# Optimization experiments

Hardware: AMD Instinct MI355X
Metric: run time of the kernel (lower is better)

## Reference

```python
import jax, jax.numpy as jnp
import numpy as np

HEAD_DIM = 512 // (8 * 2)  # in_dim // (num_heads * 2) = 32
SQRT2 = np.sqrt(2.0).astype(np.float32)


def dwt1d_haar(x):
    # Haar DWT along last dim: L=(even+odd)/sqrt2, H=(even-odd)/sqrt2
    xe, xo = x[..., 0::2], x[..., 1::2]
    return (xe + xo) / SQRT2, (xe - xo) / SQRT2


def idwt1d_haar(L, H):
    # Inverse: even=(L+H)/sqrt2, odd=(L-H)/sqrt2, interleaved
    even = (L + H) / SQRT2
    odd = (L - H) / SQRT2
    x = jnp.stack([even, odd], axis=-1)  # [..., D/2, 2]
    return x.reshape(*x.shape[:-2], -1)  # [..., D]


def setup_inputs() -> dict:
    key = jax.random.key(0)
    k1, k2, k3, k4 = jax.random.split(key, 4)
    B, S, D = 8, 2048, 512
    queries = jax.random.normal(k1, (B, S, D), dtype=jnp.float32)
    keys = jax.random.normal(k2, (B, S, D), dtype=jnp.float32)
    values = jax.random.normal(k3, (B, S, D), dtype=jnp.float32)
    W_o = jax.random.normal(k4, (D, D), dtype=jnp.float32) * (1.0 / np.sqrt(D))
    b_o = jnp.zeros((D,), dtype=jnp.float32)
    return {"queries": queries, "keys": keys, "values": values, "W_o": W_o, "b_o": b_o}


def reference(queries, keys, values, W_o, b_o):
    scale = 1.0 / jnp.sqrt(jnp.asarray(HEAD_DIM, dtype=queries.dtype))
    q_L, q_H = dwt1d_haar(queries)
    k_L, k_H = dwt1d_haar(keys)
    v_L, v_H = dwt1d_haar(values)
    # [B,S,S] score matrices for each wavelet branch
    attn_L = jax.nn.softmax(jnp.einsum("bqd,bkd->bqk", q_L, k_L) * scale, axis=-1)
    attn_H = jax.nn.softmax(jnp.einsum("bqd,bkd->bqk", q_H, k_H) * scale, axis=-1)
    L_out = jnp.einsum("bqk,bkd->bqd", attn_L, v_L)
    H_out = jnp.einsum("bqk,bkd->bqd", attn_H, v_H)
    output = idwt1d_haar(L_out, H_out)  # [B,S,D]
    return output @ W_o.T + b_o
```

## Files before the change

kernel.cpp:

```cpp
#include <hip/hip_runtime.h>

#define INV_SQRT2 0.70710678118654752f
#define QSCALE    0.17677669529663689f
#define LOG2E     1.44269504088896340f
#define SM_SHIFT  32.0f

typedef __attribute__((ext_vector_type(8))) short bf16x8;
typedef __attribute__((ext_vector_type(4))) float f32x4;
typedef __attribute__((ext_vector_type(16))) float f32x16;

__device__ __forceinline__ unsigned pack2bf(float a, float b) {
  union { float f; unsigned u; } ua, ub; ua.f = a; ub.f = b;
  unsigned ra = ua.u + 0x7FFFu + ((ua.u >> 16) & 1u);
  unsigned rb = ub.u + 0x7FFFu + ((ub.u >> 16) & 1u);
  return __builtin_amdgcn_perm(rb, ra, 0x07060302);
}

__device__ __forceinline__ float exp2_raw(float x) {
  float r;
  asm("v_exp_f32 %0, %1" : "=v"(r) : "v"(x));
  return r;
}

__device__ __forceinline__ void async16(const short* g, short* l) {
  typedef __attribute__((address_space(3))) unsigned lds_u32;
  typedef const __attribute__((address_space(1))) unsigned glb_u32;
  __builtin_amdgcn_global_load_lds((glb_u32*)g, (lds_u32*)l, 16, 0, 0);
}

__global__ void dwt_all(const float* __restrict__ q, const float* __restrict__ k,
                        const float* __restrict__ v, const float* __restrict__ W,
                        short* __restrict__ qs, short* __restrict__ ks,
                        short* __restrict__ vt, short* __restrict__ w2) {
  __shared__ float tL[64][65];
  __shared__ float tH[64][65];
  int bi = blockIdx.x;
  int t = threadIdx.x;
  if (bi < 2048) {
    int idx = bi * 256 + t;
    int j = idx & 31;
    int s = (idx >> 5) & 2047;
    int b = idx >> 16;
    const float4* qp = (const float4*)(q + ((size_t)(b * 2048 + s)) * 512 + j * 16);
    const float4* kp = (const float4*)(k + ((size_t)(b * 2048 + s)) * 512 + j * 16);
    float4 a0 = qp[0], a1 = qp[1], a2 = qp[2], a3 = qp[3];
    float4 c0 = kp[0], c1 = kp[1], c2 = kp[2], c3 = kp[3];
    union { bf16x8 v; unsigned u[4]; } qL, qH, kL, kH;
    const float cs = INV_SQRT2 * QSCALE * LOG2E;
    qL.u[0] = pack2bf((a0.x + a0.y) * cs, (a0.z + a0.w) * cs);
    qL.u[1] = pack2bf((a1.x + a1.y) * cs, (a1.z + a1.w) * cs);
    qL.u[2] = pack2bf((a2.x + a2.y) * cs, (a2.z + a2.w) * cs);
    qL.u[3] = pack2bf((a3.x + a3.y) * cs, (a3.z + a3.w) * cs);
    qH.u[0] = pack2bf((a0.x - a0.y) * cs, (a0.z - a0.w) * cs);
    qH.u[1] = pack2bf((a1.x - a1.y) * cs, (a1.z - a1.w) * cs);
    qH.u[2] = pack2bf((a2.x - a2.y) * cs, (a2.z - a2.w) * cs);
    qH.u[3] = pack2bf((a3.x - a3.y) * cs, (a3.z - a3.w) * cs);
    kL.u[0] = pack2bf((c0.x + c0.y) * INV_SQRT2, (c0.z + c0.w) * INV_SQRT2);
    kL.u[1] = pack2bf((c1.x + c1.y) * INV_SQRT2, (c1.z + c1.w) * INV_SQRT2);
    kL.u[2] = pack2bf((c2.x + c2.y) * INV_SQRT2, (c2.z + c2.w) * INV_SQRT2);
    kL.u[3] = pack2bf((c3.x + c3.y) * INV_SQRT2, (c3.z + c3.w) * INV_SQRT2);
    kH.u[0] = pack2bf((c0.x - c0.y) * INV_SQRT2, (c0.z - c0.w) * INV_SQRT2);
    kH.u[1] = pack2bf((c1.x - c1.y) * INV_SQRT2, (c1.z - c1.w) * INV_SQRT2);
    kH.u[2] = pack2bf((c2.x - c2.y) * INV_SQRT2, (c2.z - c2.w) * INV_SQRT2);
    kH.u[3] = pack2bf((c3.x - c3.y) * INV_SQRT2, (c3.z - c3.w) * INV_SQRT2);
    size_t oL = ((size_t)(b * 2) * 2048 + s) * 256 + j * 8;
    size_t oH = oL + (size_t)2048 * 256;
    *(bf16x8*)(qs + oL) = qL.v;  *(bf16x8*)(qs + oH) = qH.v;
    *(bf16x8*)(ks + oL) = kL.v;  *(bf16x8*)(ks + oH) = kH.v;
  } else if (bi < 3072) {
    int bi2 = bi - 2048;
    int it = bi2 & 3, st = (bi2 >> 2) & 31, b = bi2 >> 7;
#pragma unroll
    for (int rep = 0; rep < 8; rep++) {
      int unit = rep * 256 + t;
      int r = unit >> 5, cp = (unit & 31) * 2;
      float4 vv = *(const float4*)(v + ((size_t)(b * 2048 + st * 64 + r)) * 512 + it * 128 + cp * 2);
      tL[r][cp]     = (vv.x + vv.y) * INV_SQRT2;
      tL[r][cp + 1] = (vv.z + vv.w) * INV_SQRT2;
      tH[r][cp]     = (vv.x - vv.y) * INV_SQRT2;
      tH[r][cp + 1] = (vv.z - vv.w) * INV_SQRT2;
    }
    __syncthreads();
#pragma unroll
    for (int rep = 0; rep < 2; rep++) {
      int unit = rep * 256 + t;
      int i = unit >> 3, cc = unit & 7;
      union { bf16x8 v; unsigned u[4]; } pL, pH;
#pragma unroll
      for (int p = 0; p < 4; p++) {
        pL.u[p] = pack2bf(tL[cc * 8 + p * 2][i], tL[cc * 8 + p * 2 + 1][i]);
        pH.u[p] = pack2bf(tH[cc * 8 + p * 2][i], tH[cc * 8 + p * 2 + 1][i]);
      }
      size_t o = ((size_t)(b * 2) * 256 + it * 64 + i) * 2048 + st * 64 + cc * 8;
      *(bf16x8*)(vt + o) = pL.v;
      *(bf16x8*)(vt + o + (size_t)256 * 2048) = pH.v;
    }
  } else {
    int idx = (bi - 3072) * 256 + t;
    int j = idx >> 6, i4 = (idx & 63) * 4;
    const float4* src = (const float4*)(W + (size_t)j * 512 + 2 * i4);
    float4 f0 = src[0], f1 = src[1];
    uint2 dl, dh;
    dl.x = pack2bf((f0.x + f0.y) * INV_SQRT2, (f0.z + f0.w) * INV_SQRT2);
    dl.y = pack2bf((f1.x + f1.y) * INV_SQRT2, (f1.z + f1.w) * INV_SQRT2);
    dh.x = pack2bf((f0.x - f0.y) * INV_SQRT2, (f0.z - f0.w) * INV_SQRT2);
    dh.y = pack2bf((f1.x - f1.y) * INV_SQRT2, (f1.z - f1.w) * INV_SQRT2);
    *(uint2*)(w2 + (size_t)j * 512 + i4) = dl;
    *(uint2*)(w2 + (size_t)j * 512 + 256 + i4) = dh;
  }
}

__launch_bounds__(256, 2)
__global__ void flash_attn(const short* __restrict__ qs, const short* __restrict__ ks,
                           const short* __restrict__ vt, short* __restrict__ os) {
  __shared__ short lds[36864];
  short* klds = lds;
  short* vlds = lds + 16384;
  short* plds = lds + 32768;

  int tid = threadIdx.x;
  int w = tid >> 6, L = tid & 63;
  int lq = L & 31, hi = L >> 5;
  int qt = w & 1, ct = w >> 1;
  int bb = blockIdx.x, qb = blockIdx.y;

  bf16x8 qf[16];
  const short* qptr = qs + (((size_t)bb * 2048) + qb * 64 + qt * 32 + lq) * 256 + hi * 8;
#pragma unroll
  for (int ksI = 0; ksI < 16; ksI++)
    qf[ksI] = *(const bf16x8*)(qptr + ksI * 16);

  f32x16 oacc[4];
#pragma unroll
  for (int mt = 0; mt < 4; mt++)
#pragma unroll
    for (int i = 0; i < 16; i++) oacc[mt][i] = 0.f;
  float l_i = 0.f;

  const short* kbase = ks + ((size_t)bb * 2048) * 256;
  const short* vbase = vt + ((size_t)bb * 256) * 2048;

  int krow = ct * 32 + lq, ksw = krow & 7;
  int qrow = qt * 32 + lq, qsw = qrow & 7;
  int sw8 = lq & 7;

  const short* kaddr[16];
#pragma unroll
  for (int i = 0; i < 16; i++)
    kaddr[i] = klds + krow * 256 + (((i << 1) | hi) ^ ksw) * 8;
  short* pwr[4];
#pragma unroll
  for (int g = 0; g < 4; g++)
    pwr[g] = plds + qrow * 64 + ((4 * ct + g) ^ qsw) * 8 + hi * 4;
  const short* prdA[4];
  const short* prdB[4];
#pragma unroll
  for (int i = 0; i < 4; i++) {
    int ch = (((i << 1) | hi) ^ sw8) * 8;
    prdA[i] = plds + lq * 64 + ch;
    prdB[i] = plds + (32 + lq) * 64 + ch;
  }
  int vch[4];
#pragma unroll
  for (int i = 0; i < 4; i++)
    vch[i] = (((i << 1) | hi) ^ sw8) * 8;
  const short* vrowp[2];
#pragma unroll
  for (int dt = 0; dt < 2; dt++)
    vrowp[dt] = vlds + (w * 64 + dt * 32 + lq) * 64;

  const short* kp[8];
  const short* vp[8];
#pragma unroll
  for (int rep = 0; rep < 8; rep++) {
    int o = w * 8 + rep;
    int r = 2 * o + (L >> 5);
    int c = (L & 31) ^ (r & 7);
    kp[rep] = kbase + r * 256 + c * 8;
    int n = 8 * o + (L >> 3);
    int cv = (L & 7) ^ (n & 7);
    vp[rep] = vbase + n * 2048 + cv * 8;
  }

#pragma unroll
  for (int rep = 0; rep < 8; rep++) {
    async16(kp[rep], klds + (w * 8 + rep) * 512);
    kp[rep] += 16384;
  }
  __syncthreads();

  for (int kt = 0; kt < 32; kt++) {
#pragma unroll
    for (int rep = 0; rep < 8; rep++) {
      async16(vp[rep], vlds + (w * 8 + rep) * 512);
      vp[rep] += 64;
    }

    f32x16 s0, s1;
#pragma unroll
    for (int i = 0; i < 16; i++) { s0[i] = 0.f; s1[i] = 0.f; }
#pragma unroll
    for (int ksI = 0; ksI < 16; ksI += 2) {
      bf16x8 kb0 = *(const bf16x8*)kaddr[ksI];
      bf16x8 kb1 = *(const bf16x8*)kaddr[ksI + 1];
      s0 = __builtin_amdgcn_mfma_f32_32x32x16_bf16(kb0, qf[ksI], s0, 0, 0, 0);
      s1 = __builtin_amdgcn_mfma_f32_32x32x16_bf16(kb1, qf[ksI + 1], s1, 0, 0, 0);
    }

    float rs = 0.f;
#pragma unroll
    for (int g = 0; g < 4; g++) {
      float p0 = exp2_raw(s0[4 * g]     + s1[4 * g]     - SM_SHIFT);
      float p1 = exp2_raw(s0[4 * g + 1] + s1[4 * g + 1] - SM_SHIFT);
      float p2 = exp2_raw(s0[4 * g + 2] + s1[4 * g + 2] - SM_SHIFT);
      float p3 = exp2_raw(s0[4 * g + 3] + s1[4 * g + 3] - SM_SHIFT);
      rs += (p0 + p1) + (p2 + p3);
      uint2 d; d.x = pack2bf(p0, p1); d.y = pack2bf(p2, p3);
      *(uint2*)pwr[g] = d;
    }
    l_i += rs;
    __syncthreads();

    if (kt < 31) {
#pragma unroll
      for (int rep = 0; rep < 8; rep++) {
        async16(kp[rep], klds + (w * 8 + rep) * 512);
        kp[rep] += 16384;
      }
    }

    bf16x8 pa[4], pb[4];
#pragma unroll
    for (int i = 0; i < 4; i++) {
      pa[i] = *(const bf16x8*)prdA[i];
      pb[i] = *(const bf16x8*)prdB[i];
    }
#pragma unroll
    for (int dt = 0; dt < 2; dt++) {
#pragma unroll
      for (int i = 0; i < 4; i++) {
        bf16x8 vb = *(const bf16x8*)(vrowp[dt] + vch[i]);
        oacc[dt * 2]     = __builtin_amdgcn_mfma_f32_32x32x16_bf16(vb, pa[i], oacc[dt * 2], 0, 0, 0);
        oacc[dt * 2 + 1] = __builtin_amdgcn_mfma_f32_32x32x16_bf16(vb, pb[i], oacc[dt * 2 + 1], 0, 0, 0);
      }
    }
    __syncthreads();
  }

  float lt = l_i + __shfl_xor(l_i, 32, 64);
  float* lbuf = (float*)plds;
  if (hi == 0) lbuf[(ct * 2 + qt) * 32 + lq] = lt;
  __syncthreads();
  float inv0 = 1.f / (lbuf[lq] + lbuf[64 + lq]);
  float inv1 = 1.f / (lbuf[32 + lq] + lbuf[96 + lq]);

#pragma unroll
  for (int ot = 0; ot < 4; ot++) {
    int qt2 = ot & 1, dt = ot >> 1;
    float inv = qt2 ? inv1 : inv0;
    int qg = qt2 * 32 + lq;
#pragma unroll
    for (int g = 0; g < 4; g++) {
      uint2 d;
      d.x = pack2bf(oacc[ot][4 * g] * inv, oacc[ot][4 * g + 1] * inv);
      d.y = pack2bf(oacc[ot][4 * g + 2] * inv, oacc[ot][4 * g + 3] * inv);
      *(uint2*)(lds + qg * 264 + w * 64 + dt * 32 + 8 * g + 4 * hi) = d;
    }
  }
  __syncthreads();
  short* obase = os + (((size_t)bb * 2048) + qb * 64) * 256;
#pragma unroll
  for (int rep = 0; rep < 8; rep++) {
    int cid = rep * 256 + tid;
    int row = cid >> 5, c = cid & 31;
    *(bf16x8*)(obase + row * 256 + c * 8) = *(const bf16x8*)(lds + row * 264 + c * 8);
  }
}

__launch_bounds__(256, 2)
__global__ void out_gemm(const short* __restrict__ os, const short* __restrict__ w2,
                         const float* __restrict__ bo, float* __restrict__ out) {
  __shared__ short alds[2][8192];
  __shared__ short blds[2][8192];
  int tid = threadIdx.x;
  int w = tid >> 6, L = tid & 63, lo = L & 15, hi = L >> 4;
  int wr = w >> 1, wc = w & 1;
  int br = blockIdx.x, bc = blockIdx.y;

  int rrow[4], rchk[4];
#pragma unroll
  for (int rep = 0; rep < 4; rep++) {
    int o = w * 4 + rep;
    int r = o * 8 + (L >> 3);
    rrow[rep] = r;
    rchk[rep] = ((L & 7) ^ (r & 7)) * 8;
  }
  int b = br >> 4;
  int s0 = (br & 15) * 128;
  const short* abase = os + ((size_t)(b * 2) * 2048 + s0) * 256;
  const short* bbase = w2 + (size_t)(bc * 128) * 512;

  f32x4 acc[4][4];
#pragma unroll
  for (int mt = 0; mt < 4; mt++)
#pragma unroll
    for (int nt = 0; nt < 4; nt++)
      acc[mt][nt] = (f32x4){0.f, 0.f, 0.f, 0.f};

  int fch[2];
#pragma unroll
  for (int kc = 0; kc < 2; kc++)
    fch[kc] = ((kc * 4 + hi) ^ (lo & 7)) * 8;

#pragma unroll
  for (int rep = 0; rep < 4; rep++) {
    async16(abase + rrow[rep] * 256 + rchk[rep], &alds[0][(w * 4 + rep) * 512] + L * 8);
    async16(bbase + rrow[rep] * 512 + rchk[rep], &blds[0][(w * 4 + rep) * 512] + L * 8);
  }
  __syncthreads();

  int p = 0;
  for (int kt = 0; kt < 8; kt++) {
    if (kt < 7) {
      int k1 = kt + 1;
      int half = k1 >> 2, i0 = (k1 & 3) * 64;
      const short* ab = abase + (size_t)half * 2048 * 256 + i0;
#pragma unroll
      for (int rep = 0; rep < 4; rep++) {
        async16(ab + rrow[rep] * 256 + rchk[rep], &alds[p ^ 1][(w * 4 + rep) * 512] + L * 8);
        async16(bbase + rrow[rep] * 512 + k1 * 64 + rchk[rep], &blds[p ^ 1][(w * 4 + rep) * 512] + L * 8);
      }
    }
    bf16x8 af[4], bfr[4];
#pragma unroll
    for (int kc = 0; kc < 2; kc++) {
#pragma unroll
      for (int mt = 0; mt < 4; mt++)
        af[mt] = *(const bf16x8*)(&alds[p][(wr * 64 + mt * 16 + lo) * 64 + fch[kc]]);
#pragma unroll
      for (int nt = 0; nt < 4; nt++)
        bfr[nt] = *(const bf16x8*)(&blds[p][(wc * 64 + nt * 16 + lo) * 64 + fch[kc]]);
#pragma unroll
      for (int mt = 0; mt < 4; mt++)
#pragma unroll
        for (int nt = 0; nt < 4; nt++)
          acc[mt][nt] = __builtin_amdgcn_mfma_f32_16x16x32_bf16(af[mt], bfr[nt], acc[mt][nt], 0, 0, 0);
    }
    __syncthreads();
    p ^= 1;
  }

#pragma unroll
  for (int nt = 0; nt < 4; nt++) {
    int cc = bc * 128 + wc * 64 + nt * 16 + lo;
    float bias = bo[cc];
#pragma unroll
    for (int mt = 0; mt < 4; mt++) {
      int rrbase = br * 128 + wr * 64 + mt * 16 + hi * 4;
#pragma unroll
      for (int r = 0; r < 4; r++)
        out[(size_t)(rrbase + r) * 512 + cc] = acc[mt][nt][r] + bias;
    }
  }
}

extern "C" void kernel_launch(void* const* d_in, const int* in_sizes, int n_in,
                              void* d_out, int out_size, void* d_ws, size_t ws_size,
                              hipStream_t stream) {
  const float* q  = (const float*)d_in[0];
  const float* k  = (const float*)d_in[1];
  const float* v  = (const float*)d_in[2];
  const float* W  = (const float*)d_in[3];
  const float* bo = (const float*)d_in[4];
  short* ws  = (short*)d_ws;
  short* qs  = ws;
  short* ksb = ws + (size_t)8  * 1024 * 1024;
  short* vtp = ws + (size_t)16 * 1024 * 1024;
  short* osb = ws + (size_t)24 * 1024 * 1024;
  short* w2  = ws + (size_t)32 * 1024 * 1024;

  dwt_all<<<3200, 256, 0, stream>>>(q, k, v, W, qs, ksb, vtp, w2);
  flash_attn<<<dim3(16, 32), 256, 0, stream>>>(qs, ksb, vtp, osb);
  out_gemm<<<dim3(128, 4), 256, 0, stream>>>(osb, w2, bo, (float*)d_out);
}
```

Before: 244.5 us.

## Use hardware bf16 pack, fold softmax shift into MFMA init, add setprio

Replaces the software round-to-nearest bf16 packing with the native v_cvt_pk_bf16_f32 instruction everywhere. The softmax shift is folded into the score accumulator initialisation, split as -16 per branch, which removes a subtract before each exp. s_setprio is raised around the MFMA loops so those waves get issue priority. The V transpose in the DWT kernel now uses smaller 32-row tiles with more blocks and launch bounds of 4, trading more launches for lower LDS use and higher occupancy.

```diff
diff --git a/kernel.cpp b/kernel.cpp
--- a/kernel.cpp
+++ b/kernel.cpp
@@ -3,17 +3,16 @@
 #define INV_SQRT2 0.70710678118654752f
 #define QSCALE    0.17677669529663689f
 #define LOG2E     1.44269504088896340f
-#define SM_SHIFT  32.0f
+#define SM_HALF   16.0f
 
 typedef __attribute__((ext_vector_type(8))) short bf16x8;
 typedef __attribute__((ext_vector_type(4))) float f32x4;
 typedef __attribute__((ext_vector_type(16))) float f32x16;
 
-__device__ __forceinline__ unsigned pack2bf(float a, float b) {
-  union { float f; unsigned u; } ua, ub; ua.f = a; ub.f = b;
-  unsigned ra = ua.u + 0x7FFFu + ((ua.u >> 16) & 1u);
-  unsigned rb = ub.u + 0x7FFFu + ((ub.u >> 16) & 1u);
-  return __builtin_amdgcn_perm(rb, ra, 0x07060302);
+__device__ __forceinline__ unsigned cvt_pk_bf16(float a, float b) {
+  unsigned r;
+  asm("v_cvt_pk_bf16_f32 %0, %1, %2" : "=v"(r) : "v"(a), "v"(b));
+  return r;
 }
 
 __device__ __forceinline__ float exp2_raw(float x) {
@@ -28,12 +27,13 @@
   __builtin_amdgcn_global_load_lds((glb_u32*)g, (lds_u32*)l, 16, 0, 0);
 }
 
+__launch_bounds__(256, 4)
 __global__ void dwt_all(const float* __restrict__ q, const float* __restrict__ k,
                         const float* __restrict__ v, const float* __restrict__ W,
                         short* __restrict__ qs, short* __restrict__ ks,
                         short* __restrict__ vt, short* __restrict__ w2) {
-  __shared__ float tL[64][65];
-  __shared__ float tH[64][65];
+  __shared__ float tL[32][65];
+  __shared__ float tH[32][65];
   int bi = blockIdx.x;
   int t = threadIdx.x;
   if (bi < 2048) {
@@ -47,64 +47,62 @@
     float4 c0 = kp[0], c1 = kp[1], c2 = kp[2], c3 = kp[3];
     union { bf16x8 v; unsigned u[4]; } qL, qH, kL, kH;
     const float cs = INV_SQRT2 * QSCALE * LOG2E;
-    qL.u[0] = pack2bf((a0.x + a0.y) * cs, (a0.z + a0.w) * cs);
-    qL.u[1] = pack2bf((a1.x + a1.y) * cs, (a1.z + a1.w) * cs);
-    qL.u[2] = pack2bf((a2.x + a2.y) * cs, (a2.z + a2.w) * cs);
-    qL.u[3] = pack2bf((a3.x + a3.y) * cs, (a3.z + a3.w) * cs);
-    qH.u[0] = pack2bf((a0.x - a0.y) * cs, (a0.z - a0.w) * cs);
-    qH.u[1] = pack2bf((a1.x - a1.y) * cs, (a1.z - a1.w) * cs);
-    qH.u[2] = pack2bf((a2.x - a2.y) * cs, (a2.z - a2.w) * cs);
-    qH.u[3] = pack2bf((a3.x - a3.y) * cs, (a3.z - a3.w) * cs);
-    kL.u[0] = pack2bf((c0.x + c0.y) * INV_SQRT2, (c0.z + c0.w) * INV_SQRT2);
-    kL.u[1] = pack2bf((c1.x + c1.y) * INV_SQRT2, (c1.z + c1.w) * INV_SQRT2);
-    kL.u[2] = pack2bf((c2.x + c2.y) * INV_SQRT2, (c2.z + c2.w) * INV_SQRT2);
-    kL.u[3] = pack2bf((c3.x + c3.y) * INV_SQRT2, (c3.z + c3.w) * INV_SQRT2);
-    kH.u[0] = pack2bf((c0.x - c0.y) * INV_SQRT2, (c0.z - c0.w) * INV_SQRT2);
-    kH.u[1] = pack2bf((c1.x - c1.y) * INV_SQRT2, (c1.z - c1.w) * INV_SQRT2);
-    kH.u[2] = pack2bf((c2.x - c2.y) * INV_SQRT2, (c2.z - c2.w) * INV_SQRT2);
-    kH.u[3] = pack2bf((c3.x - c3.y) * INV_SQRT2, (c3.z - c3.w) * INV_SQRT2);
+    qL.u[0] = cvt_pk_bf16((a0.x + a0.y) * cs, (a0.z + a0.w) * cs);
+    qL.u[1] = cvt_pk_bf16((a1.x + a1.y) * cs, (a1.z + a1.w) * cs);
+    qL.u[2] = cvt_pk_bf16((a2.x + a2.y) * cs, (a2.z + a2.w) * cs);
+    qL.u[3] = cvt_pk_bf16((a3.x + a3.y) * cs, (a3.z + a3.w) * cs);
+    qH.u[0] = cvt_pk_bf16((a0.x - a0.y) * cs, (a0.z - a0.w) * cs);
+    qH.u[1] = cvt_pk_bf16((a1.x - a1.y) * cs, (a1.z - a1.w) * cs);
+    qH.u[2] = cvt_pk_bf16((a2.x - a2.y) * cs, (a2.z - a2.w) * cs);
+    qH.u[3] = cvt_pk_bf16((a3.x - a3.y) * cs, (a3.z - a3.w) * cs);
+    kL.u[0] = cvt_pk_bf16((c0.x + c0.y) * INV_SQRT2, (c0.z + c0.w) * INV_SQRT2);
+    kL.u[1] = cvt_pk_bf16((c1.x + c1.y) * INV_SQRT2, (c1.z + c1.w) * INV_SQRT2);
+    kL.u[2] = cvt_pk_bf16((c2.x + c2.y) * INV_SQRT2, (c2.z + c2.w) * INV_SQRT2);
+    kL.u[3] = cvt_pk_bf16((c3.x + c3.y) * INV_SQRT2, (c3.z + c3.w) * INV_SQRT2);
+    kH.u[0] = cvt_pk_bf16((c0.x - c0.y) * INV_SQRT2, (c0.z - c0.w) * INV_SQRT2);
+    kH.u[1] = cvt_pk_bf16((c1.x - c1.y) * INV_SQRT2, (c1.z - c1.w) * INV_SQRT2);
+    kH.u[2] = cvt_pk_bf16((c2.x - c2.y) * INV_SQRT2, (c2.z - c2.w) * INV_SQRT2);
+    kH.u[3] = cvt_pk_bf16((c3.x - c3.y) * INV_SQRT2, (c3.z - c3.w) * INV_SQRT2);
     size_t oL = ((size_t)(b * 2) * 2048 + s) * 256 + j * 8;
     size_t oH = oL + (size_t)2048 * 256;
     *(bf16x8*)(qs + oL) = qL.v;  *(bf16x8*)(qs + oH) = qH.v;
     *(bf16x8*)(ks + oL) = kL.v;  *(bf16x8*)(ks + oH) = kH.v;
-  } else if (bi < 3072) {
+  } else if (bi < 4096) {
     int bi2 = bi - 2048;
-    int it = bi2 & 3, st = (bi2 >> 2) & 31, b = bi2 >> 7;
-#pragma unroll
-    for (int rep = 0; rep < 8; rep++) {
+    int it = bi2 & 3, st = (bi2 >> 2) & 63, b = bi2 >> 8;
+#pragma unroll
+    for (int rep = 0; rep < 4; rep++) {
       int unit = rep * 256 + t;
       int r = unit >> 5, cp = (unit & 31) * 2;
-      float4 vv = *(const float4*)(v + ((size_t)(b * 2048 + st * 64 + r)) * 512 + it * 128 + cp * 2);
+      float4 vv = *(const float4*)(v + ((size_t)(b * 2048 + st * 32 + r)) * 512 + it * 128 + cp * 2);
       tL[r][cp]     = (vv.x + vv.y) * INV_SQRT2;
       tL[r][cp + 1] = (vv.z + vv.w) * INV_SQRT2;
       tH[r][cp]     = (vv.x - vv.y) * INV_SQRT2;
       tH[r][cp + 1] = (vv.z - vv.w) * INV_SQRT2;
     }
     __syncthreads();
-#pragma unroll
-    for (int rep = 0; rep < 2; rep++) {
-      int unit = rep * 256 + t;
-      int i = unit >> 3, cc = unit & 7;
+    {
+      int i = t >> 2, cc = t & 3;
       union { bf16x8 v; unsigned u[4]; } pL, pH;
 #pragma unroll
       for (int p = 0; p < 4; p++) {
-        pL.u[p] = pack2bf(tL[cc * 8 + p * 2][i], tL[cc * 8 + p * 2 + 1][i]);
-        pH.u[p] = pack2bf(tH[cc * 8 + p * 2][i], tH[cc * 8 + p * 2 + 1][i]);
+        pL.u[p] = cvt_pk_bf16(tL[cc * 8 + p * 2][i], tL[cc * 8 + p * 2 + 1][i]);
+        pH.u[p] = cvt_pk_bf16(tH[cc * 8 + p * 2][i], tH[cc * 8 + p * 2 + 1][i]);
       }
-      size_t o = ((size_t)(b * 2) * 256 + it * 64 + i) * 2048 + st * 64 + cc * 8;
+      size_t o = ((size_t)(b * 2) * 256 + it * 64 + i) * 2048 + st * 32 + cc * 8;
       *(bf16x8*)(vt + o) = pL.v;
       *(bf16x8*)(vt + o + (size_t)256 * 2048) = pH.v;
     }
   } else {
-    int idx = (bi - 3072) * 256 + t;
+    int idx = (bi - 4096) * 256 + t;
     int j = idx >> 6, i4 = (idx & 63) * 4;
     const float4* src = (const float4*)(W + (size_t)j * 512 + 2 * i4);
     float4 f0 = src[0], f1 = src[1];
     uint2 dl, dh;
-    dl.x = pack2bf((f0.x + f0.y) * INV_SQRT2, (f0.z + f0.w) * INV_SQRT2);
-    dl.y = pack2bf((f1.x + f1.y) * INV_SQRT2, (f1.z + f1.w) * INV_SQRT2);
-    dh.x = pack2bf((f0.x - f0.y) * INV_SQRT2, (f0.z - f0.w) * INV_SQRT2);
-    dh.y = pack2bf((f1.x - f1.y) * INV_SQRT2, (f1.z - f1.w) * INV_SQRT2);
+    dl.x = cvt_pk_bf16((f0.x + f0.y) * INV_SQRT2, (f0.z + f0.w) * INV_SQRT2);
+    dl.y = cvt_pk_bf16((f1.x + f1.y) * INV_SQRT2, (f1.z + f1.w) * INV_SQRT2);
+    dh.x = cvt_pk_bf16((f0.x - f0.y) * INV_SQRT2, (f0.z - f0.w) * INV_SQRT2);
+    dh.y = cvt_pk_bf16((f1.x - f1.y) * INV_SQRT2, (f1.z - f1.w) * INV_SQRT2);
     *(uint2*)(w2 + (size_t)j * 512 + i4) = dl;
     *(uint2*)(w2 + (size_t)j * 512 + 256 + i4) = dh;
   }
@@ -198,7 +196,8 @@
 
     f32x16 s0, s1;
 #pragma unroll
-    for (int i = 0; i < 16; i++) { s0[i] = 0.f; s1[i] = 0.f; }
+    for (int i = 0; i < 16; i++) { s0[i] = -SM_HALF; s1[i] = -SM_HALF; }
+    __builtin_amdgcn_s_setprio(1);
 #pragma unroll
     for (int ksI = 0; ksI < 16; ksI += 2) {
       bf16x8 kb0 = *(const bf16x8*)kaddr[ksI];
@@ -206,16 +205,17 @@
       s0 = __builtin_amdgcn_mfma_f32_32x32x16_bf16(kb0, qf[ksI], s0, 0, 0, 0);
       s1 = __builtin_amdgcn_mfma_f32_32x32x16_bf16(kb1, qf[ksI + 1], s1, 0, 0, 0);
     }
+    __builtin_amdgcn_s_setprio(0);
 
     float rs = 0.f;
 #pragma unroll
     for (int g = 0; g < 4; g++) {
-      float p0 = exp2_raw(s0[4 * g]     + s1[4 * g]     - SM_SHIFT);
-      float p1 = exp2_raw(s0[4 * g + 1] + s1[4 * g + 1] - SM_SHIFT);
-      float p2 = exp2_raw(s0[4 * g + 2] + s1[4 * g + 2] - SM_SHIFT);
-      float p3 = exp2_raw(s0[4 * g + 3] + s1[4 * g + 3] - SM_SHIFT);
+      float p0 = exp2_raw(s0[4 * g]     + s1[4 * g]);
+      float p1 = exp2_raw(s0[4 * g + 1] + s1[4 * g + 1]);
+      float p2 = exp2_raw(s0[4 * g + 2] + s1[4 * g + 2]);
+      float p3 = exp2_raw(s0[4 * g + 3] + s1[4 * g + 3]);
       rs += (p0 + p1) + (p2 + p3);
-      uint2 d; d.x = pack2bf(p0, p1); d.y = pack2bf(p2, p3);
+      uint2 d; d.x = cvt_pk_bf16(p0, p1); d.y = cvt_pk_bf16(p2, p3);
       *(uint2*)pwr[g] = d;
     }
     l_i += rs;
@@ -235,6 +235,7 @@
       pa[i] = *(const bf16x8*)prdA[i];
       pb[i] = *(const bf16x8*)prdB[i];
     }
+    __builtin_amdgcn_s_setprio(1);
 #pragma unroll
     for (int dt = 0; dt < 2; dt++) {
 #pragma unroll
@@ -244,6 +245,7 @@
         oacc[dt * 2 + 1] = __builtin_amdgcn_mfma_f32_32x32x16_bf16(vb, pb[i], oacc[dt * 2 + 1], 0, 0, 0);
       }
     }
+    __builtin_amdgcn_s_setprio(0);
     __syncthreads();
   }
 
@@ -262,8 +264,8 @@
 #pragma unroll
     for (int g = 0; g < 4; g++) {
       uint2 d;
-      d.x = pack2bf(oacc[ot][4 * g] * inv, oacc[ot][4 * g + 1] * inv);
-      d.y = pack2bf(oacc[ot][4 * g + 2] * inv, oacc[ot][4 * g + 3] * inv);
+      d.x = cvt_pk_bf16(oacc[ot][4 * g] * inv, oacc[ot][4 * g + 1] * inv);
+      d.y = cvt_pk_bf16(oacc[ot][4 * g + 2] * inv, oacc[ot][4 * g + 3] * inv);
       *(uint2*)(lds + qg * 264 + w * 64 + dt * 32 + 8 * g + 4 * hi) = d;
     }
   }
@@ -379,7 +381,7 @@
   short* osb = ws + (size_t)24 * 1024 * 1024;
   short* w2  = ws + (size_t)32 * 1024 * 1024;
 
-  dwt_all<<<3200, 256, 0, stream>>>(q, k, v, W, qs, ksb, vtp, w2);
+  dwt_all<<<4224, 256, 0, stream>>>(q, k, v, W, qs, ksb, vtp, w2);
   flash_attn<<<dim3(16, 32), 256, 0, stream>>>(qs, ksb, vtp, osb);
   out_gemm<<<dim3(128, 4), 256, 0, stream>>>(osb, w2, bo, (float*)d_out);
 }
```

New measurement: 245.3 us. No clear change (+0.3%).
